# Kernel tuning notes

Hardware: AMD Instinct MI355X
Metric: run time of the kernel (lower is better)

The kernel has to match this reference:

```python
import jax, jax.numpy as jnp
import numpy as np

B, S, D, H = 4, 2048, 512, 8
KD = D // H          # key_dim == head_dim == 64
FFN = 4 * D

def _ln(x, g, b, eps):
    mu = x.mean(-1, keepdims=True)
    var = ((x - mu) ** 2).mean(-1, keepdims=True)
    return (x - mu) / jnp.sqrt(var + eps) * g + b

def setup_inputs():
    key = jax.random.key(0)
    ks = jax.random.split(key, 8)
    def lin(k, o, i, scale=0.02):
        k1, k2 = jax.random.split(k)
        return (jax.random.normal(k1, (o, i), jnp.float32) * scale,
                jax.random.normal(k2, (o,), jnp.float32) * scale)
    wq, bq = lin(ks[0], D, D)
    wk, bk = lin(ks[1], D, D)
    wv, bv = lin(ks[2], D, D)
    wg, bg = lin(ks[3], D, D)
    wo, bo = lin(ks[4], D, D)
    fc1_w, fc1_b = lin(ks[5], FFN, D)
    fc2_w, fc2_b = lin(ks[6], D, FFN)
    return {
        'src': jax.random.normal(ks[7], (B, S, D), jnp.float32),
        'mask': jnp.zeros((S, S), jnp.bool_),
        'padding_mask': jnp.zeros((B, S), jnp.bool_),
        'wq': wq, 'bq': bq, 'wk': wk, 'bk': bk, 'wv': wv, 'bv': bv,
        'wg': wg, 'bg': bg, 'wo': wo, 'bo': bo,
        'fc1_w': fc1_w, 'fc1_b': fc1_b, 'fc2_w': fc2_w, 'fc2_b': fc2_b,
        'ln_ffn_g': jnp.ones((FFN,), jnp.float32), 'ln_ffn_b': jnp.zeros((FFN,), jnp.float32),
        'n0_g': jnp.ones((D,), jnp.float32), 'n0_b': jnp.zeros((D,), jnp.float32),
        'n1_g': jnp.ones((D,), jnp.float32), 'n1_b': jnp.zeros((D,), jnp.float32),
    }

def reference(src, mask, padding_mask, wq, bq, wk, bk, wv, bv, wg, bg, wo, bo,
              fc1_w, fc1_b, fc2_w, fc2_b, ln_ffn_g, ln_ffn_b, n0_g, n0_b, n1_g, n1_b):
    b, s, d = src.shape
    # RetNet per-head decay mask (h, s, s): exp((i-j)*log(gamma_h)) on the lower triangle,
    # row-normalized by sqrt(row sum) (torchscale RetNetRelPos, parallel mode).
    idx = jnp.arange(s)
    diff = (idx[:, None] - idx[None, :]).astype(src.dtype)
    decay = jnp.log(1.0 - 2.0 ** (-5.0 - jnp.arange(H, dtype=src.dtype)))
    dm = jnp.where(diff[None] >= 0, jnp.exp(diff[None] * decay[:, None, None]), 0.0)
    dm = dm / jnp.sqrt(dm.sum(-1, keepdims=True))
    # projections; k scaled by key_dim**-0.5 before head split
    q = (src @ wq.T + bq).reshape(b, s, H, KD).transpose(0, 2, 1, 3)
    k = ((src @ wk.T + bk) * (KD ** -0.5)).reshape(b, s, H, KD).transpose(0, 2, 1, 3)
    v = src @ wv.T + bv
    g = src @ wg.T + bg
    # parallel retention: additive decay bias, detached L1 row normalization
    qk = jnp.einsum('bhid,bhjd->bhij', q, k) + dm[None]
    den = jnp.maximum(jnp.abs(jax.lax.stop_gradient(qk).sum(-1, keepdims=True)), 1.0)
    qk = qk / den
    vr = v.reshape(b, s, H, KD).transpose(0, 2, 1, 3)
    o = jnp.einsum('bhij,bhjd->bhid', qk, vr).transpose(0, 2, 1, 3)  # (b,s,h,hd)
    # per-head LayerNorm, eps=1e-6, no affine
    mu = o.mean(-1, keepdims=True)
    o = (o - mu) / jnp.sqrt(((o - mu) ** 2).mean(-1, keepdims=True) + 1e-6)
    o = jax.nn.silu(g) * o.reshape(b, s, d)
    o = o @ wo.T + bo
    # post-norm residual layout
    x = _ln(src + o, n0_g, n0_b, 1e-5)
    h = jax.nn.gelu(x @ fc1_w.T + fc1_b, approximate=False)
    h = _ln(h, ln_ffn_g, ln_ffn_b, 1e-6)  # subln
    h = h @ fc2_w.T + fc2_b
    return _ln(x + h, n1_g, n1_b, 1e-5)
```

## Files before the change

### kernel.cpp

```cpp
#include <hip/hip_runtime.h>
#include <hip/hip_bf16.h>
#include <math.h>

#define DEV __device__ __forceinline__

typedef __attribute__((ext_vector_type(4))) float f32x4;
typedef __attribute__((ext_vector_type(16))) float f32x16;
typedef __attribute__((ext_vector_type(8))) short bf16x8;
typedef __attribute__((ext_vector_type(8))) unsigned short u16x8;
typedef unsigned short u16;
typedef unsigned int u32;
typedef __attribute__((ext_vector_type(4))) u32 u32x4;

DEV u16 f2bf(float f) {
  union { float f; u32 u; } v; v.f = f;
  u32 r = v.u + 0x7fffu + ((v.u >> 16) & 1u);
  return (u16)(r >> 16);
}
DEV float bf2f(u16 h) {
  union { u32 u; float f; } v; v.u = ((u32)h) << 16;
  return v.f;
}

DEV void gl_lds16(const u16* g, u16* s) {
  __builtin_amdgcn_global_load_lds((const __attribute__((address_space(1))) void*)g,
                                   (__attribute__((address_space(3))) void*)s, 16, 0, 0);
}

DEV u32 cvt_pk_bf16(float lo, float hi) {
  u32 r;
  asm("v_cvt_pk_bf16_f32 %0, %1, %2" : "=v"(r) : "v"(lo), "v"(hi));
  return r;
}

DEV bf16x8 u4_to_bf8(u32x4 x) {
  union { u32x4 a; bf16x8 b; } u; u.a = x; return u.b;
}

#define MFMA16(a, b, c) __builtin_amdgcn_mfma_f32_16x16x32_bf16((a), (b), (c), 0, 0, 0)
#define MFMA32(a, b, c) __builtin_amdgcn_mfma_f32_32x32x16_bf16((a), (b), (c), 0, 0, 0)

DEV void cast8(const float* in, u16* out, float s) {
  f32x4 a = *(const f32x4*)in;
  f32x4 b = *(const f32x4*)(in + 4);
  u16x8 r;
  r[0] = f2bf(a[0] * s); r[1] = f2bf(a[1] * s); r[2] = f2bf(a[2] * s); r[3] = f2bf(a[3] * s);
  r[4] = f2bf(b[0] * s); r[5] = f2bf(b[1] * s); r[6] = f2bf(b[2] * s); r[7] = f2bf(b[3] * s);
  *(u16x8*)out = r;
}

__global__ __launch_bounds__(256) void prep_cast(
    const float* __restrict__ src, const float* __restrict__ wq, const float* __restrict__ wk,
    const float* __restrict__ wv, const float* __restrict__ wg, const float* __restrict__ wo,
    const float* __restrict__ fc1, const float* __restrict__ fc2,
    const float* __restrict__ bq, const float* __restrict__ bk,
    const float* __restrict__ bv, const float* __restrict__ bg,
    u16* __restrict__ src_bf, u16* __restrict__ Wcat, u16* __restrict__ wo_bf,
    u16* __restrict__ fc1_bf, u16* __restrict__ fc2_bf, float* __restrict__ bcat) {
  int u = blockIdx.x * 256 + threadIdx.x;
  if (u < 524288) {
    cast8(src + (size_t)u * 8, src_bf + (size_t)u * 8, 1.0f);
  } else if (u < 557056) {
    int v = u - 524288; cast8(wq + (size_t)v * 8, Wcat + (size_t)v * 8, 1.0f);
  } else if (u < 589824) {
    int v = u - 557056; cast8(wk + (size_t)v * 8, Wcat + 262144 + (size_t)v * 8, 0.125f);
  } else if (u < 622592) {
    int v = u - 589824; cast8(wv + (size_t)v * 8, Wcat + 524288 + (size_t)v * 8, 1.0f);
  } else if (u < 655360) {
    int v = u - 622592; cast8(wg + (size_t)v * 8, Wcat + 786432 + (size_t)v * 8, 1.0f);
  } else if (u < 688128) {
    int v = u - 655360; cast8(wo + (size_t)v * 8, wo_bf + (size_t)v * 8, 1.0f);
  } else if (u < 819200) {
    int v = u - 688128; cast8(fc1 + (size_t)v * 8, fc1_bf + (size_t)v * 8, 1.0f);
  } else if (u < 950272) {
    int v = u - 819200; cast8(fc2 + (size_t)v * 8, fc2_bf + (size_t)v * 8, 1.0f);
  } else if (u < 950528) {
    int v = u - 950272;
    #pragma unroll
    for (int e = 0; e < 8; e++) {
      int c = v * 8 + e;
      float val;
      if (c < 512)       val = bq[c];
      else if (c < 1024) val = bk[c - 512] * 0.125f;
      else if (c < 1536) val = bv[c - 1024];
      else               val = bg[c - 1536];
      bcat[c] = val;
    }
  }
}

template <int ACT>
__global__ __launch_bounds__(256) void gemm_v3(
    const u16* __restrict__ A, const u16* __restrict__ W, const float* __restrict__ bias,
    u16* __restrict__ Ob, int N, int K, int TN) {
  __shared__ __align__(16) u16 sm[2][16384];
  const int t = threadIdx.x, l = t & 63;
  const int w = t >> 6, wr = (w >> 1) * 64, wc = (w & 1) * 64;
  const int lc = l & 15, lch = l >> 4;
  const int NT = K >> 6;

  const int orig = blockIdx.x;
  const int cpx = gridDim.x >> 3;
  const int sid = (orig & 7) * cpx + (orig >> 3);
  const int bm = (sid / TN) * 128, bn = (sid % TN) * 128;

  const int srow = t >> 3, sc8 = t & 7;
  const u16* stA = A + (size_t)(bm + srow) * K + ((sc8 ^ (srow & 7)) * 8);
  const u16* stB = W + (size_t)(bn + srow) * K + ((sc8 ^ (srow & 7)) * 8);

#define STAGE(bidx, kt)                                                        \
  {                                                                            \
    u16* d = (u16*)sm[bidx] + t * 8;                                           \
    _Pragma("unroll")                                                          \
    for (int j = 0; j < 4; j++)                                                \
      gl_lds16(stA + (size_t)j * 32 * K + (kt), d + j * 2048);                 \
    _Pragma("unroll")                                                          \
    for (int j = 0; j < 4; j++)                                                \
      gl_lds16(stB + (size_t)j * 32 * K + (kt), d + 8192 + j * 2048);          \
  }

  f32x4 acc[4][4] = {};

  STAGE(0, 0)
  __syncthreads();

  for (int tt = 0; tt < NT; ++tt) {
    if (tt + 1 < NT) STAGE((tt + 1) & 1, (tt + 1) * 64)
    const u16* bufp = sm[tt & 1];
    bf16x8 af[4][2], bfv[4][2];
    #pragma unroll
    for (int mi = 0; mi < 4; mi++) {
      const int row = wr + mi * 16 + lc;
      #pragma unroll
      for (int ks = 0; ks < 2; ks++) {
        const int ch = ks * 4 + lch;
        af[mi][ks] = *(const bf16x8*)&bufp[row * 64 + ((ch ^ (row & 7)) * 8)];
      }
    }
    #pragma unroll
    for (int ni = 0; ni < 4; ni++) {
      const int row = wc + ni * 16 + lc;
      #pragma unroll
      for (int ks = 0; ks < 2; ks++) {
        const int ch = ks * 4 + lch;
        bfv[ni][ks] = *(const bf16x8*)&bufp[8192 + row * 64 + ((ch ^ (row & 7)) * 8)];
      }
    }
    #pragma unroll
    for (int ks = 0; ks < 2; ks++)
      #pragma unroll
      for (int mi = 0; mi < 4; mi++)
        #pragma unroll
        for (int ni = 0; ni < 4; ni++)
          acc[mi][ni] = MFMA16(af[mi][ks], bfv[ni][ks], acc[mi][ni]);
    __syncthreads();
  }
#undef STAGE

  u16* osm = (u16*)sm;
  #pragma unroll
  for (int ni = 0; ni < 4; ni++) {
    const int col = wc + ni * 16 + lc;
    const float bb = bias[bn + col];
    const int ckey = col >> 3, clow = col & 7;
    #pragma unroll
    for (int mi = 0; mi < 4; mi++) {
      #pragma unroll
      for (int r = 0; r < 4; r++) {
        const int row = wr + mi * 16 + lch * 4 + r;
        float v = acc[mi][ni][r] + bb;
        if (ACT == 1) v = 0.5f * v * (1.0f + erff(v * 0.70710678118f));
        osm[row * 128 + ((ckey ^ ((row & 7) << 1)) << 3) + clow] = f2bf(v);
      }
    }
  }
  __syncthreads();
  #pragma unroll
  for (int p = 0; p < 8; p++) {
    const int flat = p * 256 + t;
    const int row = flat >> 4, c = flat & 15;
    u16x8 y = *(const u16x8*)&osm[row * 128 + ((c ^ ((row & 7) << 1)) << 3)];
    *(u16x8*)&Ob[(size_t)(bm + row) * N + bn + c * 8] = y;
  }
}

__global__ __launch_bounds__(512) void retention_v2(
    const u16* __restrict__ qkvg, u16* __restrict__ gated) {
  const int S = 2048, DD = 2048;
  const int bh = blockIdx.y, b = bh >> 3, h = bh & 7;
  const int t = threadIdx.x, l = t & 63, w = t >> 6;
  const int lid = l & 31, hi = l >> 5;
  const int wrow = blockIdx.x * 256 + w * 32;
  const int i_q = wrow + lid;

  __shared__ __align__(16) u16 sm[18432];

  const size_t base = (size_t)b * S * DD + (size_t)h * 64;
  const u16* qp = qkvg + base;
  const u16* kp = qkvg + base + 512;
  const u16* vp = qkvg + base + 1024;
  const u16* gp = qkvg + base + 1536;

  const float gamma = 1.0f - exp2f(-5.0f - (float)h);
  const float l2g = log2f(gamma);
  const float rowsum = (1.0f - exp2f((float)(i_q + 1) * l2g)) * exp2f(5.0f + (float)h);
  const float ai = exp2f((float)i_q * l2g) * rsqrtf(rowsum);
  float bjc[16];
  #pragma unroll
  for (int r = 0; r < 16; r++) {
    int joff = (r & 3) + 8 * (r >> 2) + 4 * hi;
    bjc[r] = exp2f(-(float)joff * l2g);
  }
  const float E32 = exp2f(-32.0f * l2g);
  const float E64 = E32 * E32;
  float Ejt = 1.0f;

  bf16x8 qf[4];
  #pragma unroll
  for (int ks = 0; ks < 4; ks++)
    qf[ks] = *(const bf16x8*)(qp + (size_t)i_q * DD + ks * 16 + 8 * hi);

  f32x16 accO0, accO1;
  #pragma unroll
  for (int r = 0; r < 16; r++) { accO0[r] = 0.0f; accO1[r] = 0.0f; }
  float den_acc = 0.0f;

  const int krow = t >> 3, kcc = t & 7;
  const u16* kg_src = kp + (size_t)krow * DD + ((kcc ^ (krow & 7)) * 8);
  const int vj = t & 63, vd0 = (t >> 6) * 8;
  const u16* vg_src = vp + (size_t)vj * DD + vd0;

  gl_lds16(kg_src, sm + t * 8);
  {
    u16x8 v0 = *(const u16x8*)vg_src;
    #pragma unroll
    for (int e = 0; e < 8; e++) sm[8192 + (vd0 + e) * 72 + vj] = v0[e];
  }
  __syncthreads();

  int cur = 0;
  for (int jt = 0; jt < S; jt += 64) {
    const int nxt = cur ^ 1;
    const bool pref = (jt + 64 < S);
    u16x8 vreg;
    if (pref) {
      vreg = *(const u16x8*)(vg_src + (size_t)(jt + 64) * DD);
      gl_lds16(kg_src + (size_t)(jt + 64) * DD, sm + nxt * 4096 + t * 8);
    }
    const u16* KsB = sm + cur * 4096;
    const u16* VtB = sm + 8192 + cur * 4608;

    #pragma unroll
    for (int jsub = 0; jsub < 2; jsub++) {
      f32x16 s;
      #pragma unroll
      for (int r = 0; r < 16; r++) s[r] = 0.0f;
      #pragma unroll
      for (int ks = 0; ks < 4; ks++) {
        bf16x8 kf = *(const bf16x8*)&KsB[(jsub * 32 + lid) * 64 +
                                         (((2 * ks + hi) ^ (lid & 7)) * 8)];
        s = MFMA32(kf, qf[ks], s);
      }
      {
        const int js = jt + jsub * 32;
        if (js + 31 <= wrow) {
          float coef = ai * Ejt * (jsub ? E32 : 1.0f);
          #pragma unroll
          for (int r = 0; r < 16; r++) s[r] += coef * bjc[r];
        } else if (js <= wrow + 31) {
          float coef = ai * Ejt * (jsub ? E32 : 1.0f);
          #pragma unroll
          for (int r = 0; r < 16; r++) {
            int j = js + (r & 3) + 8 * (r >> 2) + 4 * hi;
            s[r] += (j <= i_q) ? coef * bjc[r] : 0.0f;
          }
        }
      }
      #pragma unroll
      for (int r = 0; r < 16; r++) den_acc += s[r];
      u32 pk[8];
      #pragma unroll
      for (int q = 0; q < 4; q++) {
        pk[q * 2 + 0] = cvt_pk_bf16(s[4 * q + 0], s[4 * q + 1]);
        pk[q * 2 + 1] = cvt_pk_bf16(s[4 * q + 2], s[4 * q + 3]);
      }
      #pragma unroll
      for (int p = 0; p < 2; p++) {
        u32 own0 = hi ? pk[(2 * p + 1) * 2 + 0] : pk[(2 * p) * 2 + 0];
        u32 own1 = hi ? pk[(2 * p + 1) * 2 + 1] : pk[(2 * p) * 2 + 1];
        u32 snd0 = hi ? pk[(2 * p) * 2 + 0] : pk[(2 * p + 1) * 2 + 0];
        u32 snd1 = hi ? pk[(2 * p) * 2 + 1] : pk[(2 * p + 1) * 2 + 1];
        u32 r0 = __shfl_xor(snd0, 32);
        u32 r1 = __shfl_xor(snd1, 32);
        u32x4 paw;
        paw[0] = hi ? r0 : own0;
        paw[1] = hi ? r1 : own1;
        paw[2] = hi ? own0 : r0;
        paw[3] = hi ? own1 : r1;
        bf16x8 paf = u4_to_bf8(paw);
        const int jsl = jsub * 2 + p;
        bf16x8 vt0 = *(const bf16x8*)&VtB[(lid) * 72 + jsl * 16 + 8 * hi];
        bf16x8 vt1 = *(const bf16x8*)&VtB[(32 + lid) * 72 + jsl * 16 + 8 * hi];
        accO0 = MFMA32(vt0, paf, accO0);
        accO1 = MFMA32(vt1, paf, accO1);
      }
    }

    if (pref) {
      #pragma unroll
      for (int e = 0; e < 8; e++)
        sm[8192 + nxt * 4608 + (vd0 + e) * 72 + vj] = vreg[e];
    }
    Ejt *= E64;
    __syncthreads();
    cur = nxt;
  }

  float den = den_acc + __shfl_xor(den_acc, 32);
  float rden = 1.0f / fmaxf(fabsf(den), 1.0f);
  float o0[16], o1[16];
  float s1 = 0.0f, s2 = 0.0f;
  #pragma unroll
  for (int r = 0; r < 16; r++) {
    o0[r] = accO0[r] * rden; s1 += o0[r]; s2 += o0[r] * o0[r];
    o1[r] = accO1[r] * rden; s1 += o1[r]; s2 += o1[r] * o1[r];
  }
  s1 += __shfl_xor(s1, 32);
  s2 += __shfl_xor(s2, 32);
  float mu = s1 * (1.0f / 64.0f);
  float var = s2 * (1.0f / 64.0f) - mu * mu;
  float rv = rsqrtf(var + 1e-6f);

  u16* Ot = sm + w * 2304;
  #pragma unroll
  for (int r = 0; r < 16; r++) {
    int d = (r & 3) + 8 * (r >> 2) + 4 * hi;
    Ot[lid * 72 + d]      = f2bf((o0[r] - mu) * rv);
    Ot[lid * 72 + 32 + d] = f2bf((o1[r] - mu) * rv);
  }
  {
    const int i2 = l >> 1, half = l & 1;
    const int row = wrow + i2;
    #pragma unroll
    for (int c = 0; c < 4; c++) {
      u16x8 y8 = *(const u16x8*)&Ot[i2 * 72 + half * 32 + c * 8];
      u16x8 g8 = *(const u16x8*)(gp + (size_t)row * DD + half * 32 + c * 8);
      u16x8 o8;
      #pragma unroll
      for (int e = 0; e < 8; e++) {
        float gv = bf2f(g8[e]);
        float sg = gv / (1.0f + __expf(-gv));
        o8[e] = f2bf(bf2f(y8[e]) * sg);
      }
      *(u16x8*)&gated[((size_t)(b * S + row)) * 512 + h * 64 + half * 32 + c * 8] = o8;
    }
  }
}

__global__ __launch_bounds__(256) void add_ln512(
    const float* __restrict__ A, const u16* __restrict__ Bv,
    const float* __restrict__ gam, const float* __restrict__ bet, float eps,
    float* __restrict__ Of, u16* __restrict__ Ob) {
  int row = blockIdx.x * 4 + (threadIdx.x >> 6);
  int l = threadIdx.x & 63;
  const float* a = A + (size_t)row * 512 + l * 8;
  f32x4 a0 = *(const f32x4*)a, a1 = *(const f32x4*)(a + 4);
  u16x8 cv = *(const u16x8*)(Bv + (size_t)row * 512 + l * 8);
  float x[8];
  #pragma unroll
  for (int e = 0; e < 4; e++) { x[e] = a0[e] + bf2f(cv[e]); x[4 + e] = a1[e] + bf2f(cv[4 + e]); }
  float s = 0.f, s2 = 0.f;
  #pragma unroll
  for (int e = 0; e < 8; e++) { s += x[e]; s2 += x[e] * x[e]; }
  #pragma unroll
  for (int m = 1; m <= 32; m <<= 1) { s += __shfl_xor(s, m); s2 += __shfl_xor(s2, m); }
  float mu = s * (1.0f / 512.0f);
  float var = s2 * (1.0f / 512.0f) - mu * mu;
  float rinv = rsqrtf(var + eps);
  f32x4 g0 = *(const f32x4*)(gam + l * 8), g1 = *(const f32x4*)(gam + l * 8 + 4);
  f32x4 b0 = *(const f32x4*)(bet + l * 8), b1 = *(const f32x4*)(bet + l * 8 + 4);
  f32x4 y0, y1;
  #pragma unroll
  for (int e = 0; e < 4; e++) {
    y0[e] = (x[e] - mu) * rinv * g0[e] + b0[e];
    y1[e] = (x[4 + e] - mu) * rinv * g1[e] + b1[e];
  }
  float* op = Of + (size_t)row * 512 + l * 8;
  *(f32x4*)op = y0;
  *(f32x4*)(op + 4) = y1;
  if (Ob) {
    u16x8 rb_;
    #pragma unroll
    for (int e = 0; e < 4; e++) { rb_[e] = f2bf(y0[e]); rb_[4 + e] = f2bf(y1[e]); }
    *(u16x8*)(Ob + (size_t)row * 512 + l * 8) = rb_;
  }
}

__global__ __launch_bounds__(256) void subln_ffn(
    u16* __restrict__ hbuf, const float* __restrict__ gam, const float* __restrict__ bet) {
  int row = blockIdx.x * 4 + (threadIdx.x >> 6);
  int l = threadIdx.x & 63;
  u16* p = hbuf + (size_t)row * 2048;
  float x[32];
  #pragma unroll
  for (int cch = 0; cch < 4; cch++) {
    u16x8 v = *(const u16x8*)(p + cch * 512 + l * 8);
    #pragma unroll
    for (int e = 0; e < 8; e++) x[cch * 8 + e] = bf2f(v[e]);
  }
  float s = 0.f, s2 = 0.f;
  #pragma unroll
  for (int e = 0; e < 32; e++) { s += x[e]; s2 += x[e] * x[e]; }
  #pragma unroll
  for (int m = 1; m <= 32; m <<= 1) { s += __shfl_xor(s, m); s2 += __shfl_xor(s2, m); }
  float mu = s * (1.0f / 2048.0f);
  float var = s2 * (1.0f / 2048.0f) - mu * mu;
  float rinv = rsqrtf(var + 1e-6f);
  #pragma unroll
  for (int cch = 0; cch < 4; cch++) {
    int col = cch * 512 + l * 8;
    f32x4 g0 = *(const f32x4*)(gam + col), g1 = *(const f32x4*)(gam + col + 4);
    f32x4 b0 = *(const f32x4*)(bet + col), b1 = *(const f32x4*)(bet + col + 4);
    u16x8 o;
    #pragma unroll
    for (int e = 0; e < 4; e++) {
      o[e]     = f2bf((x[cch * 8 + e]     - mu) * rinv * g0[e] + b0[e]);
      o[4 + e] = f2bf((x[cch * 8 + 4 + e] - mu) * rinv * g1[e] + b1[e]);
    }
    *(u16x8*)(p + col) = o;
  }
}

extern "C" void kernel_launch(void* const* d_in, const int* in_sizes, int n_in,
                              void* d_out, int out_size, void* d_ws, size_t ws_size,
                              hipStream_t stream) {
  const float* src  = (const float*)d_in[0];
  const float* wq   = (const float*)d_in[3];
  const float* bq   = (const float*)d_in[4];
  const float* wk   = (const float*)d_in[5];
  const float* bk   = (const float*)d_in[6];
  const float* wv   = (const float*)d_in[7];
  const float* bv   = (const float*)d_in[8];
  const float* wg   = (const float*)d_in[9];
  const float* bg   = (const float*)d_in[10];
  const float* wo   = (const float*)d_in[11];
  const float* bo   = (const float*)d_in[12];
  const float* fc1w = (const float*)d_in[13];
  const float* fc1b = (const float*)d_in[14];
  const float* fc2w = (const float*)d_in[15];
  const float* fc2b = (const float*)d_in[16];
  const float* lng  = (const float*)d_in[17];
  const float* lnb  = (const float*)d_in[18];
  const float* n0g  = (const float*)d_in[19];
  const float* n0b  = (const float*)d_in[20];
  const float* n1g  = (const float*)d_in[21];
  const float* n1b  = (const float*)d_in[22];

  if (ws_size < 90710016u) return;

  char* ws = (char*)d_ws;
  u16*   src_bf = (u16*)(ws + 0);
  u16*   Wcat   = (u16*)(ws + 8388608);
  u16*   wo_bf  = (u16*)(ws + 10485760);
  u16*   fc1_bf = (u16*)(ws + 11010048);
  u16*   fc2_bf = (u16*)(ws + 13107200);
  float* bcat   = (float*)(ws + 15204352);
  u16*   qkvg   = (u16*)(ws + 15212544);
  u16*   gated  = (u16*)(ws + 48766976);
  u16*   attn   = (u16*)(ws + 57155584);
  float* xf     = (float*)(ws + 65544192);
  u16*   xbf    = (u16*)(ws + 82321408);

  prep_cast<<<3713, 256, 0, stream>>>(src, wq, wk, wv, wg, wo, fc1w, fc2w,
                                      bq, bk, bv, bg,
                                      src_bf, Wcat, wo_bf, fc1_bf, fc2_bf, bcat);
  gemm_v3<0><<<1024, 256, 0, stream>>>(src_bf, Wcat, bcat, qkvg, 2048, 512, 16);
  retention_v2<<<dim3(8, 32), 512, 0, stream>>>(qkvg, gated);
  gemm_v3<0><<<256, 256, 0, stream>>>(gated, wo_bf, bo, attn, 512, 512, 4);
  add_ln512<<<2048, 256, 0, stream>>>(src, attn, n0g, n0b, 1e-5f, xf, xbf);
  gemm_v3<1><<<1024, 256, 0, stream>>>(xbf, fc1_bf, fc1b, qkvg, 2048, 512, 16);
  subln_ffn<<<2048, 256, 0, stream>>>(qkvg, lng, lnb);
  gemm_v3<0><<<256, 256, 0, stream>>>(qkvg, fc2_bf, fc2b, attn, 512, 2048, 4);
  add_ln512<<<2048, 256, 0, stream>>>(xf, attn, n1g, n1b, 1e-5f, (float*)d_out, nullptr);
}
```

Before: 190.2 us.

## Split retention key range across warp groups, pre-transpose V, add 64-row GEMM

Adds a separate kernel that transposes V per head into a contiguous buffer, so the retention kernel can stage both K and V tiles with direct async global-to-LDS loads into a 4-slot ring. The retention kernel now uses 128-query blocks (512 blocks instead of 256), with two warp groups each taking alternate key tiles; their partial outputs and denominators are reduced through LDS. The decay coefficient is recomputed per sub-tile with exp2 instead of carried multiplicatively. A new 64-row-tile GEMM variant replaces the N=512 output and fc2 projections to double block count, at the cost of an extra launch, a transpose pass and more LDS per block.

```diff
diff --git a/kernel.cpp b/kernel.cpp
--- a/kernel.cpp
+++ b/kernel.cpp
@@ -184,36 +184,147 @@
   }
 }
 
-__global__ __launch_bounds__(512) void retention_v2(
-    const u16* __restrict__ qkvg, u16* __restrict__ gated) {
+template <int ACT>
+__global__ __launch_bounds__(256) void gemm_m64(
+    const u16* __restrict__ A, const u16* __restrict__ W, const float* __restrict__ bias,
+    u16* __restrict__ Ob, int N, int K, int TN) {
+  __shared__ __align__(16) u16 sm[2][12288];
+  const int t = threadIdx.x, l = t & 63;
+  const int w = t >> 6, wr = (w >> 1) * 32, wc = (w & 1) * 64;
+  const int lc = l & 15, lch = l >> 4;
+  const int NT = K >> 6;
+
+  const int orig = blockIdx.x;
+  const int cpx = gridDim.x >> 3;
+  const int sid = (orig & 7) * cpx + (orig >> 3);
+  const int bm = (sid / TN) * 64, bn = (sid % TN) * 128;
+
+  const int srow = t >> 3, sc8 = t & 7;
+  const u16* stA = A + (size_t)(bm + srow) * K + ((sc8 ^ (srow & 7)) * 8);
+  const u16* stB = W + (size_t)(bn + srow) * K + ((sc8 ^ (srow & 7)) * 8);
+
+#define STAGE(bidx, kt)                                                        \
+  {                                                                            \
+    u16* d = (u16*)sm[bidx] + t * 8;                                           \
+    _Pragma("unroll")                                                          \
+    for (int j = 0; j < 2; j++)                                                \
+      gl_lds16(stA + (size_t)j * 32 * K + (kt), d + j * 2048);                 \
+    _Pragma("unroll")                                                          \
+    for (int j = 0; j < 4; j++)                                                \
+      gl_lds16(stB + (size_t)j * 32 * K + (kt), d + 4096 + j * 2048);          \
+  }
+
+  f32x4 acc[2][4] = {};
+
+  STAGE(0, 0)
+  __syncthreads();
+
+  for (int tt = 0; tt < NT; ++tt) {
+    if (tt + 1 < NT) STAGE((tt + 1) & 1, (tt + 1) * 64)
+    const u16* bufp = sm[tt & 1];
+    bf16x8 af[2][2], bfv[4][2];
+    #pragma unroll
+    for (int mi = 0; mi < 2; mi++) {
+      const int row = wr + mi * 16 + lc;
+      #pragma unroll
+      for (int ks = 0; ks < 2; ks++) {
+        const int ch = ks * 4 + lch;
+        af[mi][ks] = *(const bf16x8*)&bufp[row * 64 + ((ch ^ (row & 7)) * 8)];
+      }
+    }
+    #pragma unroll
+    for (int ni = 0; ni < 4; ni++) {
+      const int row = wc + ni * 16 + lc;
+      #pragma unroll
+      for (int ks = 0; ks < 2; ks++) {
+        const int ch = ks * 4 + lch;
+        bfv[ni][ks] = *(const bf16x8*)&bufp[4096 + row * 64 + ((ch ^ (row & 7)) * 8)];
+      }
+    }
+    #pragma unroll
+    for (int ks = 0; ks < 2; ks++)
+      #pragma unroll
+      for (int mi = 0; mi < 2; mi++)
+        #pragma unroll
+        for (int ni = 0; ni < 4; ni++)
+          acc[mi][ni] = MFMA16(af[mi][ks], bfv[ni][ks], acc[mi][ni]);
+    __syncthreads();
+  }
+#undef STAGE
+
+  u16* osm = (u16*)sm;
+  #pragma unroll
+  for (int ni = 0; ni < 4; ni++) {
+    const int col = wc + ni * 16 + lc;
+    const float bb = bias[bn + col];
+    const int ckey = col >> 3, clow = col & 7;
+    #pragma unroll
+    for (int mi = 0; mi < 2; mi++) {
+      #pragma unroll
+      for (int r = 0; r < 4; r++) {
+        const int row = wr + mi * 16 + lch * 4 + r;
+        float v = acc[mi][ni][r] + bb;
+        if (ACT == 1) v = 0.5f * v * (1.0f + erff(v * 0.70710678118f));
+        osm[row * 128 + ((ckey ^ ((row & 7) << 1)) << 3) + clow] = f2bf(v);
+      }
+    }
+  }
+  __syncthreads();
+  #pragma unroll
+  for (int p = 0; p < 4; p++) {
+    const int flat = p * 256 + t;
+    const int row = flat >> 4, c = flat & 15;
+    u16x8 y = *(const u16x8*)&osm[row * 128 + ((c ^ ((row & 7) << 1)) << 3)];
+    *(u16x8*)&Ob[(size_t)(bm + row) * N + bn + c * 8] = y;
+  }
+}
+
+__global__ __launch_bounds__(256) void vtrans(
+    const u16* __restrict__ qkvg, u16* __restrict__ vtg) {
+  __shared__ u16 L[64 * 72];
+  const int t = threadIdx.x;
+  const int jt = blockIdx.x * 64, bh = blockIdx.y, b = bh >> 3, h = bh & 7;
+  const u16* src = qkvg + (size_t)(b * 2048 + jt) * 2048 + 1024 + h * 64;
+  const int r0 = t >> 3, c0 = (t & 7) * 8;
+  u16x8 a0 = *(const u16x8*)(src + (size_t)r0 * 2048 + c0);
+  u16x8 a1 = *(const u16x8*)(src + (size_t)(r0 + 32) * 2048 + c0);
+  #pragma unroll
+  for (int e = 0; e < 8; e++) {
+    L[(c0 + e) * 72 + r0] = a0[e];
+    L[(c0 + e) * 72 + 32 + r0] = a1[e];
+  }
+  __syncthreads();
+  u16* dst = vtg + (size_t)bh * 64 * 2048 + jt;
+  *(u16x8*)(dst + (size_t)r0 * 2048 + c0) = *(const u16x8*)&L[r0 * 72 + c0];
+  *(u16x8*)(dst + (size_t)(r0 + 32) * 2048 + c0) = *(const u16x8*)&L[(r0 + 32) * 72 + c0];
+}
+
+__global__ __launch_bounds__(512, 4) void retention_v3(
+    const u16* __restrict__ qkvg, const u16* __restrict__ vtg, u16* __restrict__ gated) {
   const int S = 2048, DD = 2048;
-  const int bh = blockIdx.y, b = bh >> 3, h = bh & 7;
+  const int bh = blockIdx.x, b = bh >> 3, h = bh & 7;
   const int t = threadIdx.x, l = t & 63, w = t >> 6;
   const int lid = l & 31, hi = l >> 5;
-  const int wrow = blockIdx.x * 256 + w * 32;
+  const int g = w >> 2, w4 = w & 3;
+  const int wrow = blockIdx.y * 128 + w4 * 32;
   const int i_q = wrow + lid;
 
-  __shared__ __align__(16) u16 sm[18432];
+  __shared__ __align__(16) u16 sm[32768];
 
   const size_t base = (size_t)b * S * DD + (size_t)h * 64;
   const u16* qp = qkvg + base;
   const u16* kp = qkvg + base + 512;
-  const u16* vp = qkvg + base + 1024;
   const u16* gp = qkvg + base + 1536;
-
-  const float gamma = 1.0f - exp2f(-5.0f - (float)h);
-  const float l2g = log2f(gamma);
-  const float rowsum = (1.0f - exp2f((float)(i_q + 1) * l2g)) * exp2f(5.0f + (float)h);
-  const float ai = exp2f((float)i_q * l2g) * rsqrtf(rowsum);
+  const u16* vtp = vtg + (size_t)bh * 64 * S;
+
+  const float l2g = log2f(1.0f - exp2f(-5.0f - (float)h));
+  const float rrs = rsqrtf((1.0f - exp2f((float)(i_q + 1) * l2g)) * exp2f(5.0f + (float)h));
   float bjc[16];
   #pragma unroll
   for (int r = 0; r < 16; r++) {
     int joff = (r & 3) + 8 * (r >> 2) + 4 * hi;
     bjc[r] = exp2f(-(float)joff * l2g);
   }
-  const float E32 = exp2f(-32.0f * l2g);
-  const float E64 = E32 * E32;
-  float Ejt = 1.0f;
 
   bf16x8 qf[4];
   #pragma unroll
@@ -225,30 +336,27 @@
   for (int r = 0; r < 16; r++) { accO0[r] = 0.0f; accO1[r] = 0.0f; }
   float den_acc = 0.0f;
 
-  const int krow = t >> 3, kcc = t & 7;
-  const u16* kg_src = kp + (size_t)krow * DD + ((kcc ^ (krow & 7)) * 8);
-  const int vj = t & 63, vd0 = (t >> 6) * 8;
-  const u16* vg_src = vp + (size_t)vj * DD + vd0;
-
-  gl_lds16(kg_src, sm + t * 8);
-  {
-    u16x8 v0 = *(const u16x8*)vg_src;
-    #pragma unroll
-    for (int e = 0; e < 8; e++) sm[8192 + (vd0 + e) * 72 + vj] = v0[e];
-  }
+  const int srow = t >> 3, sc = t & 7;
+  const u16* kg = kp + (size_t)srow * DD + ((sc ^ (srow & 7)) * 8);
+  const u16* vg = vtp + (size_t)srow * S + ((sc ^ (srow & 7)) * 8);
+
+#define RSTG(tile)                                                   \
+  {                                                                  \
+    const int sl_ = (tile) & 3;                                      \
+    gl_lds16(kg + (size_t)(tile) * 64 * DD, sm + sl_ * 4096 + t * 8);\
+    gl_lds16(vg + (tile) * 64, sm + 16384 + sl_ * 4096 + t * 8);     \
+  }
+
+  RSTG(0)
+  RSTG(1)
   __syncthreads();
 
-  int cur = 0;
-  for (int jt = 0; jt < S; jt += 64) {
-    const int nxt = cur ^ 1;
-    const bool pref = (jt + 64 < S);
-    u16x8 vreg;
-    if (pref) {
-      vreg = *(const u16x8*)(vg_src + (size_t)(jt + 64) * DD);
-      gl_lds16(kg_src + (size_t)(jt + 64) * DD, sm + nxt * 4096 + t * 8);
-    }
-    const u16* KsB = sm + cur * 4096;
-    const u16* VtB = sm + 8192 + cur * 4608;
+  for (int m = 0; m < 16; ++m) {
+    if (m < 15) { RSTG(2 * m + 2) RSTG(2 * m + 3) }
+    const int tile = 2 * m + g;
+    const int jt = tile * 64;
+    const u16* KsB = sm + (tile & 3) * 4096;
+    const u16* VtB = sm + 16384 + (tile & 3) * 4096;
 
     #pragma unroll
     for (int jsub = 0; jsub < 2; jsub++) {
@@ -263,16 +371,18 @@
       }
       {
         const int js = jt + jsub * 32;
-        if (js + 31 <= wrow) {
-          float coef = ai * Ejt * (jsub ? E32 : 1.0f);
-          #pragma unroll
-          for (int r = 0; r < 16; r++) s[r] += coef * bjc[r];
-        } else if (js <= wrow + 31) {
-          float coef = ai * Ejt * (jsub ? E32 : 1.0f);
-          #pragma unroll
-          for (int r = 0; r < 16; r++) {
-            int j = js + (r & 3) + 8 * (r >> 2) + 4 * hi;
-            s[r] += (j <= i_q) ? coef * bjc[r] : 0.0f;
+        if (js <= wrow + 31) {
+          float bcoef = exp2f((float)(i_q - js) * l2g) * rrs;
+          if (js + 31 <= wrow) {
+            #pragma unroll
+            for (int r = 0; r < 16; r++) s[r] += bcoef * bjc[r];
+          } else {
+            const int dmax = i_q - js;
+            #pragma unroll
+            for (int r = 0; r < 16; r++) {
+              int joff = (r & 3) + 8 * (r >> 2) + 4 * hi;
+              s[r] += (joff <= dmax) ? bcoef * bjc[r] : 0.0f;
+            }
           }
         }
       }
@@ -299,22 +409,28 @@
         paw[3] = hi ? own1 : r1;
         bf16x8 paf = u4_to_bf8(paw);
         const int jsl = jsub * 2 + p;
-        bf16x8 vt0 = *(const bf16x8*)&VtB[(lid) * 72 + jsl * 16 + 8 * hi];
-        bf16x8 vt1 = *(const bf16x8*)&VtB[(32 + lid) * 72 + jsl * 16 + 8 * hi];
+        bf16x8 vt0 = *(const bf16x8*)&VtB[lid * 64 + (((2 * jsl + hi) ^ (lid & 7)) * 8)];
+        bf16x8 vt1 = *(const bf16x8*)&VtB[(32 + lid) * 64 + (((2 * jsl + hi) ^ (lid & 7)) * 8)];
         accO0 = MFMA32(vt0, paf, accO0);
         accO1 = MFMA32(vt1, paf, accO1);
       }
     }
-
-    if (pref) {
-      #pragma unroll
-      for (int e = 0; e < 8; e++)
-        sm[8192 + nxt * 4608 + (vd0 + e) * 72 + vj] = vreg[e];
-    }
-    Ejt *= E64;
     __syncthreads();
-    cur = nxt;
-  }
+  }
+#undef RSTG
+
+  float* red = (float*)sm;
+  const int ridx = (w4 * 64 + l) * 33;
+  if (w >= 4) {
+    #pragma unroll
+    for (int r = 0; r < 16; r++) { red[ridx + r] = accO0[r]; red[ridx + 16 + r] = accO1[r]; }
+    red[ridx + 32] = den_acc;
+  }
+  __syncthreads();
+  if (w >= 4) return;
+  #pragma unroll
+  for (int r = 0; r < 16; r++) { accO0[r] += red[ridx + r]; accO1[r] += red[ridx + 16 + r]; }
+  den_acc += red[ridx + 32];
 
   float den = den_acc + __shfl_xor(den_acc, 32);
   float rden = 1.0f / fmaxf(fabsf(den), 1.0f);
@@ -331,7 +447,7 @@
   float var = s2 * (1.0f / 64.0f) - mu * mu;
   float rv = rsqrtf(var + 1e-6f);
 
-  u16* Ot = sm + w * 2304;
+  u16* Ot = sm + 16896 + w4 * 2304;
   #pragma unroll
   for (int r = 0; r < 16; r++) {
     int d = (r & 3) + 8 * (r >> 2) + 4 * hi;
@@ -470,16 +586,18 @@
   u16*   attn   = (u16*)(ws + 57155584);
   float* xf     = (float*)(ws + 65544192);
   u16*   xbf    = (u16*)(ws + 82321408);
+  u16*   vtg    = (u16*)(ws + 65544192);
 
   prep_cast<<<3713, 256, 0, stream>>>(src, wq, wk, wv, wg, wo, fc1w, fc2w,
                                       bq, bk, bv, bg,
                                       src_bf, Wcat, wo_bf, fc1_bf, fc2_bf, bcat);
   gemm_v3<0><<<1024, 256, 0, stream>>>(src_bf, Wcat, bcat, qkvg, 2048, 512, 16);
-  retention_v2<<<dim3(8, 32), 512, 0, stream>>>(qkvg, gated);
-  gemm_v3<0><<<256, 256, 0, stream>>>(gated, wo_bf, bo, attn, 512, 512, 4);
+  vtrans<<<dim3(32, 32), 256, 0, stream>>>(qkvg, vtg);
+  retention_v3<<<dim3(32, 16), 512, 0, stream>>>(qkvg, vtg, gated);
+  gemm_m64<0><<<512, 256, 0, stream>>>(gated, wo_bf, bo, attn, 512, 512, 4);
   add_ln512<<<2048, 256, 0, stream>>>(src, attn, n0g, n0b, 1e-5f, xf, xbf);
   gemm_v3<1><<<1024, 256, 0, stream>>>(xbf, fc1_bf, fc1b, qkvg, 2048, 512, 16);
   subln_ffn<<<2048, 256, 0, stream>>>(qkvg, lng, lnb);
-  gemm_v3<0><<<256, 256, 0, stream>>>(qkvg, fc2_bf, fc2b, attn, 512, 2048, 4);
+  gemm_m64<0><<<512, 256, 0, stream>>>(qkvg, fc2_bf, fc2b, attn, 512, 2048, 4);
   add_ln512<<<2048, 256, 0, stream>>>(xf, attn, n1g, n1b, 1e-5f, (float*)d_out, nullptr);
 }
```

After: 205.2 us. 1.08x slower.
